# Kernel tuning notes

Measured on AMD Instinct MI355X. Metric: run time of the kernel, lower is better.

## Reference

```python
import jax, jax.numpy as jnp
import numpy as np

BATCH, SEQ, H, P, N, L = 8, 8192, 16, 64, 64, 64  # batch, seq, heads, d_head, d_state, block_len


def setup_inputs() -> dict:
    key = jax.random.key(0)
    k1, k2, k3 = jax.random.split(key, 3)
    X = jax.random.normal(k1, (BATCH, SEQ, H, P), dtype=jnp.float32)
    # A is the log-decay; scale down so exp(cumsum) stays finite over 8192 steps
    A = jax.random.normal(k2, (BATCH, SEQ, H), dtype=jnp.float32) * 0.02
    B = jax.random.normal(k3, (BATCH, SEQ, H, N), dtype=jnp.float32)
    return {"X": X, "A": A, "B": B}


def reference(X, A, B):
    b, s, h, p = X.shape
    n = B.shape[-1]
    l = L
    c = s // l  # n_chunks

    Xb = X.reshape(b, c, l, h, p)                      # (b,c,l,h,p)
    Ab = A.reshape(b, c, l, h).transpose(0, 3, 1, 2)   # (b,h,c,l)
    Bb = B.reshape(b, c, l, h, n)                      # (b,c,l,h,n)

    # intra-chunk cumulative decay
    A_cs = jnp.cumsum(Ab, axis=-1)                     # (b,h,c,l)
    decay_states = jnp.exp(A_cs[..., -1:] - A_cs)      # (b,h,c,l)

    # per-chunk state: sum_l decay * B outer X -> (b,c,h,p,n)
    states = jnp.einsum('bhcl,bclhn,bclhp->bchpn', decay_states, Bb, Xb)

    # prepend zero initial state
    init = jnp.zeros((b, 1, h, p, n), dtype=X.dtype)
    all_states = jnp.concatenate([init, states], axis=1)  # (b,c+1,h,p,n)

    # cross-chunk decay-weighted combination into final state
    A_ends = A_cs[..., -1]                                # (b,h,c)
    A_pad_cs = jnp.cumsum(jnp.pad(A_ends, ((0, 0), (0, 0), (1, 0))), axis=-1)  # (b,h,c+1)
    decay_chunk = jnp.exp(A_pad_cs[..., -1:] - A_pad_cs)  # (b,h,c+1)

    final_states = jnp.einsum('bhc,bchpn->bhpn', decay_chunk, all_states)  # (b,h,p,n)
    return final_states
```

## Files before the change

kernel.cpp:

```cpp
#include <hip/hip_runtime.h>

#define BATCH 8
#define SEQ   8192
#define NH    16
#define DP    64
#define ROWF  (NH*DP)
#define HGRP  4
#define NTHR  512
#define KT    32
#define RS    257

typedef __attribute__((ext_vector_type(8))) short bf16x8;
typedef __attribute__((ext_vector_type(4))) float f32x4;

static __device__ __forceinline__ unsigned pk2(float lo, float hi) {
    unsigned a = __builtin_bit_cast(unsigned, lo);
    unsigned b = __builtin_bit_cast(unsigned, hi);
    a = (a + 0x7FFFu + ((a >> 16) & 1u)) >> 16;
    b = (b + 0x7FFFu + ((b >> 16) & 1u)) & 0xFFFF0000u;
    return (a & 0xFFFFu) | b;
}

template<int NBLK>
__global__ __launch_bounds__(NTHR)
void k_partial(const float* __restrict__ Xg, const float* __restrict__ Ag,
               const float* __restrict__ Bg, float* __restrict__ part,
               float* __restrict__ blockA)
{
    constexpr int TB  = SEQ / NBLK;
    constexpr int Q   = TB / 64;
    constexpr int NKT = TB / KT;

    __shared__ unsigned XL[16][RS];
    __shared__ unsigned BL[16][RS];
    __shared__ float    WT[HGRP][TB];

    const int gid  = blockIdx.x;
    const int blk  = gid % NBLK;
    const int hg   = (gid / NBLK) & 3;
    const int b    = gid / (4 * NBLK);
    const int tid  = threadIdx.x;
    const int w    = tid >> 6;
    const int lane = tid & 63;
    const int hloc = w >> 1;
    const int nh   = w & 1;
    const int h    = hg * HGRP + hloc;
    const int t0   = blk * TB;

    float c[Q];
    {
        const size_t abase = ((size_t)(b * SEQ + t0 + lane * Q)) * NH + h;
        float run = 0.f;
        #pragma unroll
        for (int k = 0; k < Q; ++k) { run += Ag[abase + (size_t)k * NH]; c[k] = run; }
    }
    float tsum = c[Q - 1], s = tsum;
    #pragma unroll
    for (int d = 1; d < 64; d <<= 1) {
        float o = __shfl_up(s, d, 64);
        if (lane >= d) s += o;
    }
    const float total = __shfl(s, 63, 64);
    const float excl  = s - tsum;
    if (nh == 0) {
        #pragma unroll
        for (int k = 0; k < Q; ++k)
            WT[hloc][lane * Q + k] = __expf(total - (excl + c[k]));
        if (lane == 63) blockA[(size_t)(b * NH + h) * NBLK + blk] = total;
    }

    f32x4 acc[4][2];
    #pragma unroll
    for (int mi = 0; mi < 4; ++mi)
        #pragma unroll
        for (int ni = 0; ni < 2; ++ni) acc[mi][ni] = (f32x4){0.f, 0.f, 0.f, 0.f};

    const int hl = lane >> 4;
    const int p4 = (lane & 15) * 4;
    const size_t gbase = (size_t)(b * SEQ + t0) * ROWF + hg * (HGRP * DP) + hl * DP + p4;

    auto issue = [&](int k, float4* lx, float4* lb) {
        if (k >= NKT) return;
        const size_t tb = gbase + (size_t)(k * KT + w * 4) * ROWF;
        #pragma unroll
        for (int i = 0; i < 4; ++i) {
            lx[i] = *(const float4*)(Xg + tb + (size_t)i * ROWF);
            lb[i] = *(const float4*)(Bg + tb + (size_t)i * ROWF);
        }
    };
    auto cwrite = [&](int k, const float4* lx, const float4* lb) {
        const int tIn = k * KT + w * 4;
        #pragma unroll
        for (int q = 0; q < 2; ++q) {
            const float w0 = WT[hl][tIn + 2 * q];
            const float w1 = WT[hl][tIn + 2 * q + 1];
            const int   tp = w * 2 + q;
            const float* x0 = (const float*)&lx[2 * q];
            const float* x1 = (const float*)&lx[2 * q + 1];
            const float* b0 = (const float*)&lb[2 * q];
            const float* b1 = (const float*)&lb[2 * q + 1];
            #pragma unroll
            for (int pp = 0; pp < 4; ++pp) {
                XL[tp][hl * 64 + p4 + pp] = pk2(x0[pp] * w0, x1[pp] * w1);
                BL[tp][hl * 64 + p4 + pp] = pk2(b0[pp], b1[pp]);
            }
        }
    };
    auto compute = [&]() {
        const int r  = lane & 15;
        const int kg = lane >> 4;
        uint4 af[4], bf[2];
        #pragma unroll
        for (int mi = 0; mi < 4; ++mi) {
            const int row = hloc * 64 + mi * 16 + r;
            af[mi].x = XL[kg * 4 + 0][row];
            af[mi].y = XL[kg * 4 + 1][row];
            af[mi].z = XL[kg * 4 + 2][row];
            af[mi].w = XL[kg * 4 + 3][row];
        }
        #pragma unroll
        for (int ni = 0; ni < 2; ++ni) {
            const int row = hloc * 64 + nh * 32 + ni * 16 + r;
            bf[ni].x = BL[kg * 4 + 0][row];
            bf[ni].y = BL[kg * 4 + 1][row];
            bf[ni].z = BL[kg * 4 + 2][row];
            bf[ni].w = BL[kg * 4 + 3][row];
        }
        #pragma unroll
        for (int mi = 0; mi < 4; ++mi) {
            const bf16x8 a = __builtin_bit_cast(bf16x8, af[mi]);
            #pragma unroll
            for (int ni = 0; ni < 2; ++ni) {
                const bf16x8 bb = __builtin_bit_cast(bf16x8, bf[ni]);
                acc[mi][ni] = __builtin_amdgcn_mfma_f32_16x16x32_bf16(
                                  a, bb, acc[mi][ni], 0, 0, 0);
            }
        }
    };

    float4 sx0[4], sb0[4], sx1[4], sb1[4];
    issue(0, sx0, sb0);
    issue(1, sx1, sb1);
    __syncthreads();

    #pragma unroll 1
    for (int k = 0; k < NKT; k += 2) {
        cwrite(k, sx0, sb0);
        issue(k + 2, sx0, sb0);
        asm volatile("s_waitcnt lgkmcnt(0)" ::: "memory");
        __builtin_amdgcn_s_barrier();
        __builtin_amdgcn_sched_barrier(0);
        compute();
        __builtin_amdgcn_s_barrier();

        cwrite(k + 1, sx1, sb1);
        issue(k + 3, sx1, sb1);
        asm volatile("s_waitcnt lgkmcnt(0)" ::: "memory");
        __builtin_amdgcn_s_barrier();
        __builtin_amdgcn_sched_barrier(0);
        compute();
        __builtin_amdgcn_s_barrier();
    }

    float* dst = part + ((size_t)(b * NH + h) * NBLK + blk) * 4096;
    {
        const int r  = lane & 15;
        const int cg = lane >> 4;
        #pragma unroll
        for (int mi = 0; mi < 4; ++mi)
            #pragma unroll
            for (int ni = 0; ni < 2; ++ni)
                #pragma unroll
                for (int rr = 0; rr < 4; ++rr)
                    dst[(mi * 16 + cg * 4 + rr) * 64 + nh * 32 + ni * 16 + r] =
                        acc[mi][ni][rr];
    }
}

__global__ void k_scales(const float* __restrict__ blockA, float* __restrict__ scale,
                         int nblk)
{
    const int bh = blockIdx.x * blockDim.x + threadIdx.x;
    if (bh < BATCH * NH) {
        float run = 0.f;
        for (int c2 = nblk - 1; c2 >= 0; --c2) {
            scale[bh * nblk + c2] = __expf(run);
            run += blockA[bh * nblk + c2];
        }
    }
}

__global__ __launch_bounds__(256)
void k_combine(const float* __restrict__ part, const float* __restrict__ scale,
               float* __restrict__ out, int nblk)
{
    const int idx = blockIdx.x * 256 + threadIdx.x;
    const int bh  = idx >> 12;
    const int e   = idx & 4095;
    float r = 0.f;
    for (int q = 0; q < nblk; ++q)
        r += scale[bh * nblk + q] * part[((size_t)bh * nblk + q) * 4096 + e];
    out[idx] = r;
}

extern "C" void kernel_launch(void* const* d_in, const int* in_sizes, int n_in,
                              void* d_out, int out_size, void* d_ws, size_t ws_size,
                              hipStream_t stream)
{
    const float* X = (const float*)d_in[0];
    const float* A = (const float*)d_in[1];
    const float* B = (const float*)d_in[2];
    float* out     = (float*)d_out;

    const size_t need32 = ((size_t)BATCH * NH * 32 * 4096 + 2ull * BATCH * NH * 32) * 4;
    const int nblk = (ws_size >= need32) ? 32 : 16;

    float* part   = (float*)d_ws;
    float* blockA = part + (size_t)BATCH * NH * nblk * 4096;
    float* scale  = blockA + (size_t)BATCH * NH * nblk;

    if (nblk == 32)
        hipLaunchKernelGGL((k_partial<32>), dim3(BATCH * 4 * 32), dim3(NTHR), 0, stream,
                           X, A, B, part, blockA);
    else
        hipLaunchKernelGGL((k_partial<16>), dim3(BATCH * 4 * 16), dim3(NTHR), 0, stream,
                           X, A, B, part, blockA);

    hipLaunchKernelGGL(k_scales, dim3(1), dim3(128), 0, stream, blockA, scale, nblk);
    hipLaunchKernelGGL(k_combine, dim3((BATCH * NH * 4096) / 256), dim3(256), 0, stream,
                       part, scale, out, nblk);
}
```

Before: 142.5 us.

## Double-buffer LDS tiles to overlap staging writes with MFMA compute

Splits the X and B shared-memory tiles into two buffers so the next tile is converted and written into one buffer while MFMAs read the other. This removes one of the two barriers per step and lets LDS writes overlap with matrix compute. The row stride padding also changes from 257 to 260, which alters the LDS bank mapping. The cost is doubled LDS use for the tiles, which may lower occupancy.

```diff
diff --git a/kernel.cpp b/kernel.cpp
--- a/kernel.cpp
+++ b/kernel.cpp
@@ -8,7 +8,7 @@
 #define HGRP  4
 #define NTHR  512
 #define KT    32
-#define RS    257
+#define RS    260
 
 typedef __attribute__((ext_vector_type(8))) short bf16x8;
 typedef __attribute__((ext_vector_type(4))) float f32x4;
@@ -31,8 +31,8 @@
     constexpr int Q   = TB / 64;
     constexpr int NKT = TB / KT;
 
-    __shared__ unsigned XL[16][RS];
-    __shared__ unsigned BL[16][RS];
+    __shared__ unsigned XL[2][16][RS];
+    __shared__ unsigned BL[2][16][RS];
     __shared__ float    WT[HGRP][TB];
 
     const int gid  = blockIdx.x;
@@ -88,7 +88,7 @@
             lb[i] = *(const float4*)(Bg + tb + (size_t)i * ROWF);
         }
     };
-    auto cwrite = [&](int k, const float4* lx, const float4* lb) {
+    auto cwrite = [&](int k, int buf, const float4* lx, const float4* lb) {
         const int tIn = k * KT + w * 4;
         #pragma unroll
         for (int q = 0; q < 2; ++q) {
@@ -101,30 +101,30 @@
             const float* b1 = (const float*)&lb[2 * q + 1];
             #pragma unroll
             for (int pp = 0; pp < 4; ++pp) {
-                XL[tp][hl * 64 + p4 + pp] = pk2(x0[pp] * w0, x1[pp] * w1);
-                BL[tp][hl * 64 + p4 + pp] = pk2(b0[pp], b1[pp]);
+                XL[buf][tp][hl * 64 + p4 + pp] = pk2(x0[pp] * w0, x1[pp] * w1);
+                BL[buf][tp][hl * 64 + p4 + pp] = pk2(b0[pp], b1[pp]);
             }
         }
     };
-    auto compute = [&]() {
+    auto compute = [&](int buf) {
         const int r  = lane & 15;
         const int kg = lane >> 4;
         uint4 af[4], bf[2];
         #pragma unroll
         for (int mi = 0; mi < 4; ++mi) {
             const int row = hloc * 64 + mi * 16 + r;
-            af[mi].x = XL[kg * 4 + 0][row];
-            af[mi].y = XL[kg * 4 + 1][row];
-            af[mi].z = XL[kg * 4 + 2][row];
-            af[mi].w = XL[kg * 4 + 3][row];
+            af[mi].x = XL[buf][kg * 4 + 0][row];
+            af[mi].y = XL[buf][kg * 4 + 1][row];
+            af[mi].z = XL[buf][kg * 4 + 2][row];
+            af[mi].w = XL[buf][kg * 4 + 3][row];
         }
         #pragma unroll
         for (int ni = 0; ni < 2; ++ni) {
             const int row = hloc * 64 + nh * 32 + ni * 16 + r;
-            bf[ni].x = BL[kg * 4 + 0][row];
-            bf[ni].y = BL[kg * 4 + 1][row];
-            bf[ni].z = BL[kg * 4 + 2][row];
-            bf[ni].w = BL[kg * 4 + 3][row];
+            bf[ni].x = BL[buf][kg * 4 + 0][row];
+            bf[ni].y = BL[buf][kg * 4 + 1][row];
+            bf[ni].z = BL[buf][kg * 4 + 2][row];
+            bf[ni].w = BL[buf][kg * 4 + 3][row];
         }
         #pragma unroll
         for (int mi = 0; mi < 4; ++mi) {
@@ -143,23 +143,25 @@
     issue(1, sx1, sb1);
     __syncthreads();
 
+    cwrite(0, 0, sx0, sb0);
+    issue(2, sx0, sb0);
+    asm volatile("s_waitcnt lgkmcnt(0)" ::: "memory");
+    __builtin_amdgcn_s_barrier();
+    __builtin_amdgcn_sched_barrier(0);
+
     #pragma unroll 1
     for (int k = 0; k < NKT; k += 2) {
-        cwrite(k, sx0, sb0);
-        issue(k + 2, sx0, sb0);
+        if (k + 1 < NKT) { cwrite(k + 1, 1, sx1, sb1); issue(k + 3, sx1, sb1); }
+        compute(0);
         asm volatile("s_waitcnt lgkmcnt(0)" ::: "memory");
         __builtin_amdgcn_s_barrier();
         __builtin_amdgcn_sched_barrier(0);
-        compute();
-        __builtin_amdgcn_s_barrier();
-
-        cwrite(k + 1, sx1, sb1);
-        issue(k + 3, sx1, sb1);
+
+        if (k + 2 < NKT) { cwrite(k + 2, 0, sx0, sb0); issue(k + 4, sx0, sb0); }
+        if (k + 1 < NKT) compute(1);
         asm volatile("s_waitcnt lgkmcnt(0)" ::: "memory");
         __builtin_amdgcn_s_barrier();
         __builtin_amdgcn_sched_barrier(0);
-        compute();
-        __builtin_amdgcn_s_barrier();
     }
 
     float* dst = part + ((size_t)(b * NH + h) * NBLK + blk) * 4096;
```

After: 145.5 us. 2.1% more time.

## Stream X and B directly into LDS via global_load_lds and convert at compute time

Applied to the files above, without the earlier changes.

Replaces register-staged global loads and the pack-and-write-to-LDS step with direct global-to-LDS DMA loads of fp32 rows into an 8-slot ring buffer. The decay weighting and bf16 packing move into the compute phase, which reads fp32 from LDS. The aim is to cut VGPR staging and the separate LDS write pass, and to overlap loads with MFMA work through a two-quad-ahead pipeline gated by vmcnt. In exchange, LDS traffic and footprint double because data is stored as fp32, and conversion work is repeated by each wave that reads the tile.

```diff
diff --git a/kernel.cpp b/kernel.cpp
--- a/kernel.cpp
+++ b/kernel.cpp
@@ -7,11 +7,12 @@
 #define ROWF  (NH*DP)
 #define HGRP  4
 #define NTHR  512
-#define KT    32
-#define RS    257
+#define RSF   257
 
 typedef __attribute__((ext_vector_type(8))) short bf16x8;
 typedef __attribute__((ext_vector_type(4))) float f32x4;
+typedef const __attribute__((address_space(1))) void* gptr_t;
+typedef __attribute__((address_space(3))) void* lptr_t;
 
 static __device__ __forceinline__ unsigned pk2(float lo, float hi) {
     unsigned a = __builtin_bit_cast(unsigned, lo);
@@ -27,13 +28,13 @@
                const float* __restrict__ Bg, float* __restrict__ part,
                float* __restrict__ blockA)
 {
-    constexpr int TB  = SEQ / NBLK;
-    constexpr int Q   = TB / 64;
-    constexpr int NKT = TB / KT;
-
-    __shared__ unsigned XL[16][RS];
-    __shared__ unsigned BL[16][RS];
-    __shared__ float    WT[HGRP][TB];
+    constexpr int TB = SEQ / NBLK;
+    constexpr int Q  = TB / 64;
+    constexpr int NQ = TB / 32;
+
+    __shared__ float XLf[8][8][RSF];
+    __shared__ float BLf[8][8][RSF];
+    __shared__ float WT[HGRP][TB];
 
     const int gid  = blockIdx.x;
     const int blk  = gid % NBLK;
@@ -75,91 +76,74 @@
         #pragma unroll
         for (int ni = 0; ni < 2; ++ni) acc[mi][ni] = (f32x4){0.f, 0.f, 0.f, 0.f};
 
-    const int hl = lane >> 4;
-    const int p4 = (lane & 15) * 4;
-    const size_t gbase = (size_t)(b * SEQ + t0) * ROWF + hg * (HGRP * DP) + hl * DP + p4;
-
-    auto issue = [&](int k, float4* lx, float4* lb) {
-        if (k >= NKT) return;
-        const size_t tb = gbase + (size_t)(k * KT + w * 4) * ROWF;
-        #pragma unroll
-        for (int i = 0; i < 4; ++i) {
-            lx[i] = *(const float4*)(Xg + tb + (size_t)i * ROWF);
-            lb[i] = *(const float4*)(Bg + tb + (size_t)i * ROWF);
+    auto issueQuad = [&](int qq) {
+        if (qq >= NQ) return;
+        #pragma unroll
+        for (int si = 0; si < 4; ++si) {
+            const int sIdx = (4 * qq + si) & 7;
+            const size_t rb = (size_t)(b * SEQ + t0 + 32 * qq + 8 * si + w) * ROWF
+                              + hg * (HGRP * DP) + lane * 4;
+            __builtin_amdgcn_global_load_lds((gptr_t)(Xg + rb),
+                                             (lptr_t)&XLf[sIdx][w][0], 16, 0, 0);
+            __builtin_amdgcn_global_load_lds((gptr_t)(Bg + rb),
+                                             (lptr_t)&BLf[sIdx][w][0], 16, 0, 0);
         }
     };
-    auto cwrite = [&](int k, const float4* lx, const float4* lb) {
-        const int tIn = k * KT + w * 4;
-        #pragma unroll
-        for (int q = 0; q < 2; ++q) {
-            const float w0 = WT[hl][tIn + 2 * q];
-            const float w1 = WT[hl][tIn + 2 * q + 1];
-            const int   tp = w * 2 + q;
-            const float* x0 = (const float*)&lx[2 * q];
-            const float* x1 = (const float*)&lx[2 * q + 1];
-            const float* b0 = (const float*)&lb[2 * q];
-            const float* b1 = (const float*)&lb[2 * q + 1];
-            #pragma unroll
-            for (int pp = 0; pp < 4; ++pp) {
-                XL[tp][hl * 64 + p4 + pp] = pk2(x0[pp] * w0, x1[pp] * w1);
-                BL[tp][hl * 64 + p4 + pp] = pk2(b0[pp], b1[pp]);
-            }
-        }
-    };
-    auto compute = [&]() {
+
+    auto computeQuad = [&](int qq) {
         const int r  = lane & 15;
         const int kg = lane >> 4;
-        uint4 af[4], bf[2];
+        const int sIdx = (4 * qq + kg) & 7;
+        float wts[8];
+        #pragma unroll
+        for (int j = 0; j < 8; ++j) wts[j] = WT[hloc][32 * qq + kg * 8 + j];
+        uint4 av[4], bv[2];
         #pragma unroll
         for (int mi = 0; mi < 4; ++mi) {
             const int row = hloc * 64 + mi * 16 + r;
-            af[mi].x = XL[kg * 4 + 0][row];
-            af[mi].y = XL[kg * 4 + 1][row];
-            af[mi].z = XL[kg * 4 + 2][row];
-            af[mi].w = XL[kg * 4 + 3][row];
+            float xs[8];
+            #pragma unroll
+            for (int j = 0; j < 8; ++j) xs[j] = XLf[sIdx][j][row] * wts[j];
+            av[mi].x = pk2(xs[0], xs[1]); av[mi].y = pk2(xs[2], xs[3]);
+            av[mi].z = pk2(xs[4], xs[5]); av[mi].w = pk2(xs[6], xs[7]);
         }
         #pragma unroll
         for (int ni = 0; ni < 2; ++ni) {
             const int row = hloc * 64 + nh * 32 + ni * 16 + r;
-            bf[ni].x = BL[kg * 4 + 0][row];
-            bf[ni].y = BL[kg * 4 + 1][row];
-            bf[ni].z = BL[kg * 4 + 2][row];
-            bf[ni].w = BL[kg * 4 + 3][row];
+            float bs[8];
+            #pragma unroll
+            for (int j = 0; j < 8; ++j) bs[j] = BLf[sIdx][j][row];
+            bv[ni].x = pk2(bs[0], bs[1]); bv[ni].y = pk2(bs[2], bs[3]);
+            bv[ni].z = pk2(bs[4], bs[5]); bv[ni].w = pk2(bs[6], bs[7]);
         }
         #pragma unroll
         for (int mi = 0; mi < 4; ++mi) {
-            const bf16x8 a = __builtin_bit_cast(bf16x8, af[mi]);
-            #pragma unroll
-            for (int ni = 0; ni < 2; ++ni) {
-                const bf16x8 bb = __builtin_bit_cast(bf16x8, bf[ni]);
+            const bf16x8 a = __builtin_bit_cast(bf16x8, av[mi]);
+            #pragma unroll
+            for (int ni = 0; ni < 2; ++ni)
                 acc[mi][ni] = __builtin_amdgcn_mfma_f32_16x16x32_bf16(
-                                  a, bb, acc[mi][ni], 0, 0, 0);
-            }
+                                  a, __builtin_bit_cast(bf16x8, bv[ni]),
+                                  acc[mi][ni], 0, 0, 0);
         }
     };
 
-    float4 sx0[4], sb0[4], sx1[4], sb1[4];
-    issue(0, sx0, sb0);
-    issue(1, sx1, sb1);
-    __syncthreads();
+    issueQuad(0);
+    issueQuad(1);
+    asm volatile("s_waitcnt lgkmcnt(0)" ::: "memory");
+    __builtin_amdgcn_s_barrier();
 
     #pragma unroll 1
-    for (int k = 0; k < NKT; k += 2) {
-        cwrite(k, sx0, sb0);
-        issue(k + 2, sx0, sb0);
+    for (int q = 0; q < NQ; ++q) {
+        if (q < NQ - 1)
+            asm volatile("s_waitcnt vmcnt(8)" ::: "memory");
+        else
+            asm volatile("s_waitcnt vmcnt(0)" ::: "memory");
+        __builtin_amdgcn_s_barrier();
+        __builtin_amdgcn_sched_barrier(0);
+        computeQuad(q);
         asm volatile("s_waitcnt lgkmcnt(0)" ::: "memory");
         __builtin_amdgcn_s_barrier();
-        __builtin_amdgcn_sched_barrier(0);
-        compute();
-        __builtin_amdgcn_s_barrier();
-
-        cwrite(k + 1, sx1, sb1);
-        issue(k + 3, sx1, sb1);
-        asm volatile("s_waitcnt lgkmcnt(0)" ::: "memory");
-        __builtin_amdgcn_s_barrier();
-        __builtin_amdgcn_sched_barrier(0);
-        compute();
-        __builtin_amdgcn_s_barrier();
+        issueQuad(q + 2);
     }
 
     float* dst = part + ((size_t)(b * NH + h) * NBLK + blk) * 4096;
```

Result: slower. 161.8 us (+13.5%).
